# Optimization experiments

Measured on AMD Instinct MI355X. Metric: run time of the kernel, lower is better.

Reference implementation:

```python
import jax, jax.numpy as jnp
import numpy as np

N, K, C, OUT = 2048, 14, 512, 512
SCALE = 4.0
BN_EPS = 1e-5


def _edge_lists(k):
    # pairs i<j with i,j != k-1 and adj[i,j] > 0 (adj is fully connected ones)
    ei, ej = [], []
    for i in range(k - 1):
        for j in range(i + 1, k - 1):
            ei.append(i)
            ej.append(j)
    return np.asarray(ei, np.int32), np.asarray(ej, np.int32)


def setup_inputs() -> dict:
    key = jax.random.key(0)
    k0, k1, k2, k3 = jax.random.split(key, 4)
    ei, ej = _edge_lists(K)
    std = 0.02
    return {
        "inputs": jax.random.normal(k0, (N, K, C), dtype=jnp.float32),
        "adj": jnp.ones((K, K), dtype=jnp.float32),
        "edge_i": jnp.asarray(ei),
        "edge_j": jnp.asarray(ej),
        "gamma": jnp.ones((C,), dtype=jnp.float32),
        "beta": jnp.zeros((C,), dtype=jnp.float32),
        "w_direct": jax.random.normal(k1, (C,), dtype=jnp.float32) * std,
        "W_merged": jax.random.normal(k2, (OUT, C), dtype=jnp.float32) * std,
        "W_orig": jax.random.normal(k3, (OUT, C), dtype=jnp.float32) * std,
    }


def reference(inputs, adj, edge_i, edge_j, gamma, beta, w_direct, W_merged, W_orig):
    n, k, c = inputs.shape
    # --- learn_adj ---
    global_feat = inputs[:, k - 1 : k, :]                      # [N,1,c]
    distances = jnp.abs(inputs - global_feat)                  # [N,k,c]
    # pairwise gaps only on the static edge list (i<j, non-global, adj>0)
    gap = 15.0 * (distances[:, edge_i, :] - distances[:, edge_j, :])  # [N,E,c]
    # BatchNorm1d over channel c, batch stats over (N, E), biased variance
    mean = jnp.mean(gap, axis=(0, 1))
    var = jnp.mean(jnp.square(gap - mean), axis=(0, 1))
    bn = (gap - mean) * (gamma / jnp.sqrt(var + BN_EPS)) + beta        # [N,E,c]
    a = jax.nn.sigmoid(SCALE * jnp.einsum("nec,c->ne", bn, w_direct))  # [N,E]
    adj2 = jnp.ones((n, k, k), dtype=inputs.dtype)
    adj2 = adj2.at[:, edge_i, edge_j].set(2.0 * a)
    adj2 = adj2.at[:, edge_j, edge_i].set(2.0 * (1.0 - a))
    new_adj = adj2 * adj[None, :, :]
    norm = jnp.sum(jnp.abs(new_adj), axis=2, keepdims=True)    # L1 row norm
    new_adj = new_adj / jnp.maximum(norm, 1e-12)
    # --- graph conv ---
    agg = jnp.einsum("nij,njc->nic", new_adj, inputs)          # [N,k,c]
    merged = jax.nn.relu(jnp.einsum("nkc,oc->nko", agg, W_merged))
    original = jnp.einsum("nkc,oc->nko", inputs, W_orig)
    return merged + original
```

## Files before the change

### kernel.cpp

```cpp
#include <hip/hip_runtime.h>
#include <stdint.h>

#define K_NODES 14
#define C_DIM   512
#define OUT_DIM 512
#define N_EDGE  78

typedef float  f32x4  __attribute__((ext_vector_type(4)));
typedef __bf16 bf16x8 __attribute__((ext_vector_type(8)));

__device__ __forceinline__ unsigned short f2bf(float f) {
    unsigned int u = __builtin_bit_cast(unsigned int, f);
    unsigned int r = (u + 0x7fffu + ((u >> 16) & 1u)) >> 16;
    return (unsigned short)r;
}
__device__ __forceinline__ float bf2f(unsigned short s) {
    return __builtin_bit_cast(float, (unsigned int)s << 16);
}

__device__ __forceinline__ void async16(const void* g, void* l) {
    __builtin_amdgcn_global_load_lds(
        (const __attribute__((address_space(1))) unsigned int*)g,
        (__attribute__((address_space(3))) unsigned int*)l, 16, 0, 0);
}

__global__ __launch_bounds__(512) void stats_partial(
    const float* __restrict__ x, float* __restrict__ part,
    unsigned short* __restrict__ xbf,
    const float* __restrict__ Wm, const float* __restrict__ Wo,
    unsigned short* __restrict__ wmbf, unsigned short* __restrict__ wobf)
{
    int t  = threadIdx.x;
    int q  = t & 127;
    int sn = t >> 7;
    f32x4 as = (f32x4){0.f,0.f,0.f,0.f};
    f32x4 aq = (f32x4){0.f,0.f,0.f,0.f};

    #pragma unroll
    for (int half = 0; half < 2; ++half) {
        int n = blockIdx.x * 8 + half * 4 + sn;
        size_t base = (size_t)n * K_NODES * C_DIM + q * 4;

        f32x4 g = *(const f32x4*)(x + base + 13 * C_DIM);
        ushort4 gb; gb.x=f2bf(g.x); gb.y=f2bf(g.y); gb.z=f2bf(g.z); gb.w=f2bf(g.w);
        *(ushort4*)(xbf + base + 13 * C_DIM) = gb;

        float S10=0,S11=0,S12=0,S13=0, S20=0,S21=0,S22=0,S23=0, Sw0=0,Sw1=0,Sw2=0,Sw3=0;
        #pragma unroll
        for (int k = 0; k < 13; ++k) {
            f32x4 v = *(const f32x4*)(x + base + k * C_DIM);
            ushort4 vb; vb.x=f2bf(v.x); vb.y=f2bf(v.y); vb.z=f2bf(v.z); vb.w=f2bf(v.w);
            *(ushort4*)(xbf + base + k * C_DIM) = vb;
            float wk = (float)(12 - 2 * k);
            float d0=fabsf(v.x-g.x), d1=fabsf(v.y-g.y), d2=fabsf(v.z-g.z), d3=fabsf(v.w-g.w);
            S10+=d0; S11+=d1; S12+=d2; S13+=d3;
            S20+=d0*d0; S21+=d1*d1; S22+=d2*d2; S23+=d3*d3;
            Sw0+=wk*d0; Sw1+=wk*d1; Sw2+=wk*d2; Sw3+=wk*d3;
        }
        as += (f32x4){15.f*Sw0, 15.f*Sw1, 15.f*Sw2, 15.f*Sw3};
        aq += (f32x4){225.f*(13.f*S20 - S10*S10), 225.f*(13.f*S21 - S11*S11),
                      225.f*(13.f*S22 - S12*S12), 225.f*(13.f*S23 - S13*S13)};
    }

    __shared__ f32x4 redS[4][128];
    __shared__ f32x4 redQ[4][128];
    redS[sn][q] = as;
    redQ[sn][q] = aq;
    __syncthreads();
    if (sn == 0) {
        f32x4 s = redS[0][q], z = redQ[0][q];
        #pragma unroll
        for (int r = 1; r < 4; ++r) { s += redS[r][q]; z += redQ[r][q]; }
        *(f32x4*)(part + (size_t)blockIdx.x * 1024 + q * 4)       = s;
        *(f32x4*)(part + (size_t)blockIdx.x * 1024 + 512 + q * 4) = z;
    }
    int i0 = blockIdx.x * 1024 + t;
    wmbf[i0] = f2bf(Wm[i0]);
    wobf[i0] = f2bf(Wo[i0]);
    wmbf[i0 + 512] = f2bf(Wm[i0 + 512]);
    wobf[i0 + 512] = f2bf(Wo[i0 + 512]);
}

__global__ __launch_bounds__(256) void finalize_stats(
    const float* __restrict__ part, float inv_ne,
    const float* __restrict__ gamma, const float* __restrict__ beta,
    const float* __restrict__ wdir, float* __restrict__ u, float* __restrict__ bpart)
{
    int lane = threadIdx.x & 63;
    int wv   = threadIdx.x >> 6;
    int c    = blockIdx.x * 64 + lane;
    float s = 0.f, q = 0.f;
    #pragma unroll 8
    for (int r = wv; r < 256; r += 4) {
        s += part[(size_t)r * 1024 + c];
        q += part[(size_t)r * 1024 + 512 + c];
    }
    __shared__ float shs[4][64], shq[4][64];
    shs[wv][lane] = s; shq[wv][lane] = q;
    __syncthreads();
    if (wv == 0) {
        s = shs[0][lane] + shs[1][lane] + shs[2][lane] + shs[3][lane];
        q = shq[0][lane] + shq[1][lane] + shq[2][lane] + shq[3][lane];
        float mean = s * inv_ne;
        float var  = q * inv_ne - mean * mean;
        float sc   = gamma[c] / sqrtf(var + 1e-5f);
        u[c] = sc * wdir[c];
        float b = (beta[c] - mean * sc) * wdir[c];
        #pragma unroll
        for (int off = 1; off < 64; off <<= 1) b += __shfl_xor(b, off, 64);
        if (lane == 0) bpart[blockIdx.x] = b;
    }
}

__global__ __launch_bounds__(256) void fuse_graph(
    const unsigned short* __restrict__ xbf, const float* __restrict__ adj,
    const int* __restrict__ ei, const int* __restrict__ ej,
    const float* __restrict__ u, const float* __restrict__ bpart,
    unsigned short* __restrict__ aggbf)
{
    __shared__ float WL[4][196];
    __shared__ float Dsh[4][13];
    __shared__ float invW[4][14];
    int wv = threadIdx.x >> 6, lane = threadIdx.x & 63;
    int n  = blockIdx.x * 4 + wv;
    size_t base = (size_t)n * K_NODES * C_DIM + lane * 8;

    float xf[K_NODES][8];
    #pragma unroll
    for (int k = 0; k < K_NODES; ++k) {
        uint4 raw = *(const uint4*)(xbf + base + k * C_DIM);
        xf[k][0]=bf2f(raw.x&0xffff); xf[k][1]=bf2f(raw.x>>16);
        xf[k][2]=bf2f(raw.y&0xffff); xf[k][3]=bf2f(raw.y>>16);
        xf[k][4]=bf2f(raw.z&0xffff); xf[k][5]=bf2f(raw.z>>16);
        xf[k][6]=bf2f(raw.w&0xffff); xf[k][7]=bf2f(raw.w>>16);
    }
    float uvv[8];
    {
        f32x4 a = *(const f32x4*)(u + lane * 8);
        f32x4 b = *(const f32x4*)(u + lane * 8 + 4);
        uvv[0]=a.x; uvv[1]=a.y; uvv[2]=a.z; uvv[3]=a.w;
        uvv[4]=b.x; uvv[5]=b.y; uvv[6]=b.z; uvv[7]=b.w;
    }

    #pragma unroll
    for (int k = 0; k < 13; ++k) {
        float p = 0.f;
        #pragma unroll
        for (int c = 0; c < 8; ++c) p += fabsf(xf[k][c]-xf[13][c])*uvv[c];
        #pragma unroll
        for (int off = 1; off < 64; off <<= 1) p += __shfl_xor(p, off, 64);
        if (lane == 0) Dsh[wv][k] = p;
    }

    #pragma unroll
    for (int r = 0; r < 4; ++r) {
        int idx = r * 64 + lane;
        if (idx < K_NODES * K_NODES) {
            int i = idx / K_NODES, j = idx - i * K_NODES;
            if (i == j || i == 13 || j == 13) WL[wv][idx] = adj[idx];
        }
    }
    float bc = 0.f;
    #pragma unroll
    for (int b8 = 0; b8 < 8; ++b8) bc += bpart[b8];
    #pragma unroll
    for (int r = 0; r < 2; ++r) {
        int e = r * 64 + lane;
        if (e < N_EDGE) {
            int ii = ei[e], jj = ej[e];
            float z = 4.0f * (15.f * (Dsh[wv][ii] - Dsh[wv][jj]) + bc);
            float a = 1.f / (1.f + expf(-z));
            WL[wv][ii * K_NODES + jj] = adj[ii * K_NODES + jj] * (2.f * a);
            WL[wv][jj * K_NODES + ii] = adj[jj * K_NODES + ii] * (2.f * (1.f - a));
        }
    }
    if (lane < K_NODES) {
        float s = 0.f;
        #pragma unroll
        for (int j = 0; j < K_NODES; ++j) s += fabsf(WL[wv][lane * K_NODES + j]);
        invW[wv][lane] = 1.f / fmaxf(s, 1e-12f);
    }

    #pragma unroll
    for (int i = 0; i < K_NODES; ++i) {
        float s0=0,s1=0,s2=0,s3=0,s4=0,s5=0,s6=0,s7=0;
        #pragma unroll
        for (int j = 0; j < K_NODES; ++j) {
            float w = WL[wv][i * K_NODES + j];
            s0+=w*xf[j][0]; s1+=w*xf[j][1]; s2+=w*xf[j][2]; s3+=w*xf[j][3];
            s4+=w*xf[j][4]; s5+=w*xf[j][5]; s6+=w*xf[j][6]; s7+=w*xf[j][7];
        }
        float wi = invW[wv][i];
        uint4 r;
        r.x = (unsigned int)f2bf(s0*wi) | ((unsigned int)f2bf(s1*wi) << 16);
        r.y = (unsigned int)f2bf(s2*wi) | ((unsigned int)f2bf(s3*wi) << 16);
        r.z = (unsigned int)f2bf(s4*wi) | ((unsigned int)f2bf(s5*wi) << 16);
        r.w = (unsigned int)f2bf(s6*wi) | ((unsigned int)f2bf(s7*wi) << 16);
        *(uint4*)(aggbf + base + i * C_DIM) = r;
    }
}

#define TM 128
#define TN 128
#define BK 64

__global__ __launch_bounds__(256) void gemm_fused(
    const unsigned short* __restrict__ Aagg, const unsigned short* __restrict__ Axin,
    const unsigned short* __restrict__ Bwm,  const unsigned short* __restrict__ Bwo,
    float* __restrict__ out)
{
    __shared__ unsigned short lA[2][TM * BK];
    __shared__ unsigned short lB[2][TN * BK];
    int tid  = threadIdx.x;
    int lane = tid & 63;
    int wave = tid >> 6;
    int wr = wave >> 1, wc = wave & 1;
    int bm = blockIdx.x * TM;
    int bn = blockIdx.y * TN;

    f32x4 acc[4][4];
    #pragma unroll
    for (int i = 0; i < 4; ++i)
        #pragma unroll
        for (int j = 0; j < 4; ++j) acc[i][j] = (f32x4){0.f, 0.f, 0.f, 0.f};

    int lrow = lane & 15;
    int xorv = lane & 7;
    int srow  = tid >> 3;
    int lcu   = ((tid & 7) ^ (srow & 7)) * 8;

#define STAGE(buf, Ap, Bp, kb)                                              \
    _Pragma("unroll")                                                        \
    for (int it = 0; it < 4; ++it) {                                         \
        int row = it * 32 + srow;                                            \
        async16((Ap) + (size_t)(bm + row) * C_DIM + (kb) + lcu,              \
                &lA[buf][(it * 256 + wave * 64) * 8]);                       \
        async16((Bp) + (size_t)(bn + row) * C_DIM + (kb) + lcu,              \
                &lB[buf][(it * 256 + wave * 64) * 8]);                       \
    }

    STAGE(0, Aagg, Bwm, 0);
    __syncthreads();

    #pragma unroll
    for (int ph = 0; ph < 16; ++ph) {
        const int cur = ph & 1;
        if (ph < 15) {
            const unsigned short* Ap = ((ph + 1) < 8) ? Aagg : Axin;
            const unsigned short* Bp = ((ph + 1) < 8) ? Bwm  : Bwo;
            STAGE(cur ^ 1, Ap, Bp, ((ph + 1) & 7) * BK);
        }
        #pragma unroll
        for (int ks = 0; ks < 2; ++ks) {
            int pchunk = ((ks * 4 + (lane >> 4)) ^ xorv) * 8;
            bf16x8 af[4], bfr[4];
            #pragma unroll
            for (int i = 0; i < 4; ++i)
                af[i] = *(const bf16x8*)&lA[cur][(wr * 64 + i * 16 + lrow) * BK + pchunk];
            #pragma unroll
            for (int j = 0; j < 4; ++j)
                bfr[j] = *(const bf16x8*)&lB[cur][(wc * 64 + j * 16 + lrow) * BK + pchunk];
            #pragma unroll
            for (int i = 0; i < 4; ++i)
                #pragma unroll
                for (int j = 0; j < 4; ++j)
                    acc[i][j] = __builtin_amdgcn_mfma_f32_16x16x32_bf16(
                        af[i], bfr[j], acc[i][j], 0, 0, 0);
        }
        if (ph == 7) {
            #pragma unroll
            for (int i = 0; i < 4; ++i)
                #pragma unroll
                for (int j = 0; j < 4; ++j)
                    #pragma unroll
                    for (int r = 0; r < 4; ++r)
                        acc[i][j][r] = fmaxf(acc[i][j][r], 0.f);
        }
        __syncthreads();
    }
#undef STAGE

    int orow0 = bm + wr * 64 + (lane >> 4) * 4;
    int ocol0 = bn + wc * 64 + (lane & 15);
    #pragma unroll
    for (int i = 0; i < 4; ++i)
        #pragma unroll
        for (int j = 0; j < 4; ++j)
            #pragma unroll
            for (int r = 0; r < 4; ++r)
                out[(size_t)(orow0 + i * 16 + r) * OUT_DIM + (ocol0 + j * 16)] = acc[i][j][r];
}

extern "C" void kernel_launch(void* const* d_in, const int* in_sizes, int n_in,
                              void* d_out, int out_size, void* d_ws, size_t ws_size,
                              hipStream_t stream)
{
    const float* x     = (const float*)d_in[0];
    const float* adj   = (const float*)d_in[1];
    const int*   ei    = (const int*)d_in[2];
    const int*   ej    = (const int*)d_in[3];
    const float* gamma = (const float*)d_in[4];
    const float* beta  = (const float*)d_in[5];
    const float* wdir  = (const float*)d_in[6];
    const float* Wm    = (const float*)d_in[7];
    const float* Wo    = (const float*)d_in[8];
    float* out = (float*)d_out;

    int N = in_sizes[0] / (K_NODES * C_DIM);
    int M = N * K_NODES;

    float* ws_f   = (float*)d_ws;
    float* u      = ws_f + 1024;
    float* bpart  = ws_f + 1536;
    float* part   = ws_f + 2048;
    char*  wsb    = (char*)d_ws;
    size_t off    = (size_t)(2048 + 256 * 1024) * sizeof(float);
    unsigned short* wmbf  = (unsigned short*)(wsb + off);  off += (size_t)OUT_DIM * C_DIM * 2;
    unsigned short* wobf  = (unsigned short*)(wsb + off);  off += (size_t)OUT_DIM * C_DIM * 2;
    unsigned short* xbf   = (unsigned short*)(wsb + off);  off += (size_t)M * C_DIM * 2;
    unsigned short* aggbf = (unsigned short*)(wsb + off);

    float inv_ne = 1.0f / ((float)N * (float)N_EDGE);

    hipLaunchKernelGGL(stats_partial, dim3(N / 8), dim3(512), 0, stream,
                       x, part, xbf, Wm, Wo, wmbf, wobf);
    hipLaunchKernelGGL(finalize_stats, dim3(8), dim3(256), 0, stream,
                       part, inv_ne, gamma, beta, wdir, u, bpart);
    hipLaunchKernelGGL(fuse_graph, dim3(N / 4), dim3(256), 0, stream,
                       xbf, adj, ei, ej, u, bpart, aggbf);
    hipLaunchKernelGGL(gemm_fused, dim3(M / TM, OUT_DIM / TN), dim3(256), 0, stream,
                       aggbf, xbf, wmbf, wobf, out);
}
```

Measured before the change: 183.0 us.

## Apply normalized adjacency after GEMM instead of materializing aggregated features

Reorders the computation so that x·W_merged^T is computed once alongside x·W_orig^T. The per-sample normalized 14x14 adjacency is then applied to the GEMM output in an epilogue before the ReLU. The gate kernel now writes only the normalized adjacency weights instead of a full bf16 aggregated-feature tensor. This removes one full activation write and read and halves the A-operand streaming in the GEMM. In exchange the GEMM uses a 112-row tile with 512 threads and about 120KB of shared memory, and adds an LDS-based epilogue for the small adjacency matmul.

```diff
diff --git a/kernel.cpp b/kernel.cpp
--- a/kernel.cpp
+++ b/kernel.cpp
@@ -112,11 +112,11 @@
     }
 }
 
-__global__ __launch_bounds__(256) void fuse_graph(
+__global__ __launch_bounds__(256) void fuse_gates(
     const unsigned short* __restrict__ xbf, const float* __restrict__ adj,
     const int* __restrict__ ei, const int* __restrict__ ej,
     const float* __restrict__ u, const float* __restrict__ bpart,
-    unsigned short* __restrict__ aggbf)
+    float* __restrict__ wfull)
 {
     __shared__ float WL[4][196];
     __shared__ float Dsh[4][13];
@@ -180,115 +180,132 @@
         for (int j = 0; j < K_NODES; ++j) s += fabsf(WL[wv][lane * K_NODES + j]);
         invW[wv][lane] = 1.f / fmaxf(s, 1e-12f);
     }
-
-    #pragma unroll
-    for (int i = 0; i < K_NODES; ++i) {
-        float s0=0,s1=0,s2=0,s3=0,s4=0,s5=0,s6=0,s7=0;
-        #pragma unroll
-        for (int j = 0; j < K_NODES; ++j) {
-            float w = WL[wv][i * K_NODES + j];
-            s0+=w*xf[j][0]; s1+=w*xf[j][1]; s2+=w*xf[j][2]; s3+=w*xf[j][3];
-            s4+=w*xf[j][4]; s5+=w*xf[j][5]; s6+=w*xf[j][6]; s7+=w*xf[j][7];
-        }
-        float wi = invW[wv][i];
-        uint4 r;
-        r.x = (unsigned int)f2bf(s0*wi) | ((unsigned int)f2bf(s1*wi) << 16);
-        r.y = (unsigned int)f2bf(s2*wi) | ((unsigned int)f2bf(s3*wi) << 16);
-        r.z = (unsigned int)f2bf(s4*wi) | ((unsigned int)f2bf(s5*wi) << 16);
-        r.w = (unsigned int)f2bf(s6*wi) | ((unsigned int)f2bf(s7*wi) << 16);
-        *(uint4*)(aggbf + base + i * C_DIM) = r;
-    }
-}
-
-#define TM 128
+    #pragma unroll
+    for (int r = 0; r < 4; ++r) {
+        int idx = r * 64 + lane;
+        if (idx < 196) {
+            int i = idx / K_NODES;
+            wfull[(size_t)n * 196 + idx] = WL[wv][idx] * invW[wv][i];
+        }
+    }
+}
+
+#define TM 112
 #define TN 128
 #define BK 64
-
-__global__ __launch_bounds__(256) void gemm_fused(
-    const unsigned short* __restrict__ Aagg, const unsigned short* __restrict__ Axin,
+#define NROW 368
+#define NISSUE 46
+
+__global__ __launch_bounds__(512, 2) void gemm_fused(
+    const unsigned short* __restrict__ Axin,
     const unsigned short* __restrict__ Bwm,  const unsigned short* __restrict__ Bwo,
+    const float* __restrict__ wfull,
     float* __restrict__ out)
 {
-    __shared__ unsigned short lA[2][TM * BK];
-    __shared__ unsigned short lB[2][TN * BK];
+    __shared__ __align__(16) char smem[122752];
+    unsigned short (*lS)[NROW * BK] = (unsigned short (*)[NROW * BK])smem;
+
     int tid  = threadIdx.x;
     int lane = tid & 63;
     int wave = tid >> 6;
-    int wr = wave >> 1, wc = wave & 1;
     int bm = blockIdx.x * TM;
     int bn = blockIdx.y * TN;
 
-    f32x4 acc[4][4];
-    #pragma unroll
-    for (int i = 0; i < 4; ++i)
-        #pragma unroll
-        for (int j = 0; j < 4; ++j) acc[i][j] = (f32x4){0.f, 0.f, 0.f, 0.f};
+    const unsigned short* gsrc[6];
+    #pragma unroll
+    for (int k = 0; k < 6; ++k) {
+        int q = wave + k * 8;
+        if (q < NISSUE) {
+            int r   = q * 8 + (lane >> 3);
+            int lch = (lane & 7) ^ (r & 7);
+            const unsigned short* s;
+            if (q < 14)      s = Axin + (size_t)(bm + r) * C_DIM;
+            else if (q < 30) s = Bwm  + (size_t)(bn + r - 112) * C_DIM;
+            else             s = Bwo  + (size_t)(bn + r - 240) * C_DIM;
+            gsrc[k] = s + lch * 8;
+        } else gsrc[k] = Axin;
+    }
+
+#define STAGE(buf, kb)                                                       \
+    _Pragma("unroll")                                                         \
+    for (int k = 0; k < 6; ++k)                                               \
+        if (wave + k * 8 < NISSUE)                                            \
+            async16(gsrc[k] + (kb), &lS[buf][(wave + k * 8) * 512]);
+
+    f32x4 accm[7], acco[7];
+    #pragma unroll
+    for (int i = 0; i < 7; ++i) {
+        accm[i] = (f32x4){0.f,0.f,0.f,0.f};
+        acco[i] = (f32x4){0.f,0.f,0.f,0.f};
+    }
 
     int lrow = lane & 15;
     int xorv = lane & 7;
-    int srow  = tid >> 3;
-    int lcu   = ((tid & 7) ^ (srow & 7)) * 8;
-
-#define STAGE(buf, Ap, Bp, kb)                                              \
-    _Pragma("unroll")                                                        \
-    for (int it = 0; it < 4; ++it) {                                         \
-        int row = it * 32 + srow;                                            \
-        async16((Ap) + (size_t)(bm + row) * C_DIM + (kb) + lcu,              \
-                &lA[buf][(it * 256 + wave * 64) * 8]);                       \
-        async16((Bp) + (size_t)(bn + row) * C_DIM + (kb) + lcu,              \
-                &lB[buf][(it * 256 + wave * 64) * 8]);                       \
-    }
-
-    STAGE(0, Aagg, Bwm, 0);
+
+    STAGE(0, 0)
     __syncthreads();
 
     #pragma unroll
-    for (int ph = 0; ph < 16; ++ph) {
-        const int cur = ph & 1;
-        if (ph < 15) {
-            const unsigned short* Ap = ((ph + 1) < 8) ? Aagg : Axin;
-            const unsigned short* Bp = ((ph + 1) < 8) ? Bwm  : Bwo;
-            STAGE(cur ^ 1, Ap, Bp, ((ph + 1) & 7) * BK);
-        }
+    for (int t = 0; t < 8; ++t) {
+        const int cur = t & 1;
+        if (t < 7) STAGE(cur ^ 1, (t + 1) * BK)
         #pragma unroll
         for (int ks = 0; ks < 2; ++ks) {
-            int pchunk = ((ks * 4 + (lane >> 4)) ^ xorv) * 8;
-            bf16x8 af[4], bfr[4];
+            int pch = ((ks * 4 + (lane >> 4)) ^ xorv) * 8;
+            bf16x8 af[7], bmf, bof;
             #pragma unroll
-            for (int i = 0; i < 4; ++i)
-                af[i] = *(const bf16x8*)&lA[cur][(wr * 64 + i * 16 + lrow) * BK + pchunk];
+            for (int i = 0; i < 7; ++i)
+                af[i] = *(const bf16x8*)&lS[cur][(i * 16 + lrow) * BK + pch];
+            bmf = *(const bf16x8*)&lS[cur][(112 + wave * 16 + lrow) * BK + pch];
+            bof = *(const bf16x8*)&lS[cur][(240 + wave * 16 + lrow) * BK + pch];
             #pragma unroll
-            for (int j = 0; j < 4; ++j)
-                bfr[j] = *(const bf16x8*)&lB[cur][(wc * 64 + j * 16 + lrow) * BK + pchunk];
-            #pragma unroll
-            for (int i = 0; i < 4; ++i)
-                #pragma unroll
-                for (int j = 0; j < 4; ++j)
-                    acc[i][j] = __builtin_amdgcn_mfma_f32_16x16x32_bf16(
-                        af[i], bfr[j], acc[i][j], 0, 0, 0);
-        }
-        if (ph == 7) {
-            #pragma unroll
-            for (int i = 0; i < 4; ++i)
-                #pragma unroll
-                for (int j = 0; j < 4; ++j)
-                    #pragma unroll
-                    for (int r = 0; r < 4; ++r)
-                        acc[i][j][r] = fmaxf(acc[i][j][r], 0.f);
+            for (int i = 0; i < 7; ++i) {
+                accm[i] = __builtin_amdgcn_mfma_f32_16x16x32_bf16(af[i], bmf, accm[i], 0,0,0);
+                acco[i] = __builtin_amdgcn_mfma_f32_16x16x32_bf16(af[i], bof, acco[i], 0,0,0);
+            }
         }
         __syncthreads();
     }
 #undef STAGE
 
-    int orow0 = bm + wr * 64 + (lane >> 4) * 4;
-    int ocol0 = bn + wc * 64 + (lane & 15);
-    #pragma unroll
-    for (int i = 0; i < 4; ++i)
-        #pragma unroll
-        for (int j = 0; j < 4; ++j)
-            #pragma unroll
-            for (int r = 0; r < 4; ++r)
-                out[(size_t)(orow0 + i * 16 + r) * OUT_DIM + (ocol0 + j * 16)] = acc[i][j][r];
+    float (*UmL)[130] = (float (*)[130])smem;
+    float (*UoL)[130] = (float (*)[130])(smem + 58240);
+    float *wsh        = (float*)(smem + 116480);
+
+    int q4 = lane >> 4, c15 = lane & 15;
+    #pragma unroll
+    for (int i = 0; i < 7; ++i)
+        #pragma unroll
+        for (int r = 0; r < 4; ++r) {
+            int row = i * 16 + q4 * 4 + r;
+            UmL[row][wave * 16 + c15] = accm[i][r];
+            UoL[row][wave * 16 + c15] = acco[i][r];
+        }
+    for (int idx = tid; idx < 8 * 196; idx += 512)
+        wsh[idx] = wfull[(size_t)blockIdx.x * 8 * 196 + idx];
+    __syncthreads();
+
+    float a0[14], a1[14];
+    #pragma unroll
+    for (int ii = 0; ii < 14; ++ii) { a0[ii] = 0.f; a1[ii] = 0.f; }
+    #pragma unroll
+    for (int j = 0; j < 14; ++j) {
+        float um0 = UmL[wave * 14 + j][lane];
+        float um1 = UmL[wave * 14 + j][lane + 64];
+        #pragma unroll
+        for (int ii = 0; ii < 14; ++ii) {
+            float wv_ = wsh[wave * 196 + ii * 14 + j];
+            a0[ii] += wv_ * um0;
+            a1[ii] += wv_ * um1;
+        }
+    }
+    #pragma unroll
+    for (int ii = 0; ii < 14; ++ii) {
+        int row = wave * 14 + ii;
+        size_t o = (size_t)(bm + row) * OUT_DIM + bn;
+        out[o + lane]      = fmaxf(a0[ii], 0.f) + UoL[row][lane];
+        out[o + lane + 64] = fmaxf(a1[ii], 0.f) + UoL[row][lane + 64];
+    }
 }
 
 extern "C" void kernel_launch(void* const* d_in, const int* in_sizes, int n_in,
@@ -318,7 +335,7 @@
     unsigned short* wmbf  = (unsigned short*)(wsb + off);  off += (size_t)OUT_DIM * C_DIM * 2;
     unsigned short* wobf  = (unsigned short*)(wsb + off);  off += (size_t)OUT_DIM * C_DIM * 2;
     unsigned short* xbf   = (unsigned short*)(wsb + off);  off += (size_t)M * C_DIM * 2;
-    unsigned short* aggbf = (unsigned short*)(wsb + off);
+    float*          wfull = (float*)(wsb + off);           off += (size_t)N * 196 * 4;
 
     float inv_ne = 1.0f / ((float)N * (float)N_EDGE);
 
@@ -326,8 +343,8 @@
                        x, part, xbf, Wm, Wo, wmbf, wobf);
     hipLaunchKernelGGL(finalize_stats, dim3(8), dim3(256), 0, stream,
                        part, inv_ne, gamma, beta, wdir, u, bpart);
-    hipLaunchKernelGGL(fuse_graph, dim3(N / 4), dim3(256), 0, stream,
-                       xbf, adj, ei, ej, u, bpart, aggbf);
-    hipLaunchKernelGGL(gemm_fused, dim3(M / TM, OUT_DIM / TN), dim3(256), 0, stream,
-                       aggbf, xbf, wmbf, wobf, out);
-}
+    hipLaunchKernelGGL(fuse_gates, dim3(N / 4), dim3(256), 0, stream,
+                       xbf, adj, ei, ej, u, bpart, wfull);
+    hipLaunchKernelGGL(gemm_fused, dim3(M / TM, OUT_DIM / TN), dim3(512), 0, stream,
+                       xbf, wmbf, wobf, wfull, out);
+}
```

After: 185.3 us. About the same (+1.2%).

## Replace stats partials and finalize kernel with atomics and in-kernel finalize

Applied to the files above, without the earlier changes.

The stats kernel now handles 4 samples per block over twice as many blocks and accumulates per-channel sums into a global buffer with float atomics, instead of writing per-block partials. The separate finalize kernel is removed. Every fuse_graph block recomputes the BN scale vector and bias from the accumulated sums into shared memory. This drops one kernel launch and the partial-buffer round trip, but adds a memset, atomic contention on 1024 addresses, redundant per-block finalize work, and order-dependent float accumulation.

```diff
diff --git a/kernel.cpp b/kernel.cpp
--- a/kernel.cpp
+++ b/kernel.cpp
@@ -25,7 +25,7 @@
 }
 
 __global__ __launch_bounds__(512) void stats_partial(
-    const float* __restrict__ x, float* __restrict__ part,
+    const float* __restrict__ x, float* __restrict__ accum,
     unsigned short* __restrict__ xbf,
     const float* __restrict__ Wm, const float* __restrict__ Wo,
     unsigned short* __restrict__ wmbf, unsigned short* __restrict__ wobf)
@@ -33,34 +33,28 @@
     int t  = threadIdx.x;
     int q  = t & 127;
     int sn = t >> 7;
-    f32x4 as = (f32x4){0.f,0.f,0.f,0.f};
-    f32x4 aq = (f32x4){0.f,0.f,0.f,0.f};
-
-    #pragma unroll
-    for (int half = 0; half < 2; ++half) {
-        int n = blockIdx.x * 8 + half * 4 + sn;
-        size_t base = (size_t)n * K_NODES * C_DIM + q * 4;
-
-        f32x4 g = *(const f32x4*)(x + base + 13 * C_DIM);
-        ushort4 gb; gb.x=f2bf(g.x); gb.y=f2bf(g.y); gb.z=f2bf(g.z); gb.w=f2bf(g.w);
-        *(ushort4*)(xbf + base + 13 * C_DIM) = gb;
-
-        float S10=0,S11=0,S12=0,S13=0, S20=0,S21=0,S22=0,S23=0, Sw0=0,Sw1=0,Sw2=0,Sw3=0;
-        #pragma unroll
-        for (int k = 0; k < 13; ++k) {
-            f32x4 v = *(const f32x4*)(x + base + k * C_DIM);
-            ushort4 vb; vb.x=f2bf(v.x); vb.y=f2bf(v.y); vb.z=f2bf(v.z); vb.w=f2bf(v.w);
-            *(ushort4*)(xbf + base + k * C_DIM) = vb;
-            float wk = (float)(12 - 2 * k);
-            float d0=fabsf(v.x-g.x), d1=fabsf(v.y-g.y), d2=fabsf(v.z-g.z), d3=fabsf(v.w-g.w);
-            S10+=d0; S11+=d1; S12+=d2; S13+=d3;
-            S20+=d0*d0; S21+=d1*d1; S22+=d2*d2; S23+=d3*d3;
-            Sw0+=wk*d0; Sw1+=wk*d1; Sw2+=wk*d2; Sw3+=wk*d3;
-        }
-        as += (f32x4){15.f*Sw0, 15.f*Sw1, 15.f*Sw2, 15.f*Sw3};
-        aq += (f32x4){225.f*(13.f*S20 - S10*S10), 225.f*(13.f*S21 - S11*S11),
-                      225.f*(13.f*S22 - S12*S12), 225.f*(13.f*S23 - S13*S13)};
-    }
+    int n  = blockIdx.x * 4 + sn;
+    size_t base = (size_t)n * K_NODES * C_DIM + q * 4;
+
+    f32x4 g = *(const f32x4*)(x + base + 13 * C_DIM);
+    ushort4 gb; gb.x=f2bf(g.x); gb.y=f2bf(g.y); gb.z=f2bf(g.z); gb.w=f2bf(g.w);
+    *(ushort4*)(xbf + base + 13 * C_DIM) = gb;
+
+    float S10=0,S11=0,S12=0,S13=0, S20=0,S21=0,S22=0,S23=0, Sw0=0,Sw1=0,Sw2=0,Sw3=0;
+    #pragma unroll
+    for (int k = 0; k < 13; ++k) {
+        f32x4 v = *(const f32x4*)(x + base + k * C_DIM);
+        ushort4 vb; vb.x=f2bf(v.x); vb.y=f2bf(v.y); vb.z=f2bf(v.z); vb.w=f2bf(v.w);
+        *(ushort4*)(xbf + base + k * C_DIM) = vb;
+        float wk = (float)(12 - 2 * k);
+        float d0=fabsf(v.x-g.x), d1=fabsf(v.y-g.y), d2=fabsf(v.z-g.z), d3=fabsf(v.w-g.w);
+        S10+=d0; S11+=d1; S12+=d2; S13+=d3;
+        S20+=d0*d0; S21+=d1*d1; S22+=d2*d2; S23+=d3*d3;
+        Sw0+=wk*d0; Sw1+=wk*d1; Sw2+=wk*d2; Sw3+=wk*d3;
+    }
+    f32x4 as = (f32x4){15.f*Sw0, 15.f*Sw1, 15.f*Sw2, 15.f*Sw3};
+    f32x4 aq = (f32x4){225.f*(13.f*S20 - S10*S10), 225.f*(13.f*S21 - S11*S11),
+                       225.f*(13.f*S22 - S12*S12), 225.f*(13.f*S23 - S13*S13)};
 
     __shared__ f32x4 redS[4][128];
     __shared__ f32x4 redQ[4][128];
@@ -68,62 +62,55 @@
     redQ[sn][q] = aq;
     __syncthreads();
     if (sn == 0) {
-        f32x4 s = redS[0][q], z = redQ[0][q];
-        #pragma unroll
-        for (int r = 1; r < 4; ++r) { s += redS[r][q]; z += redQ[r][q]; }
-        *(f32x4*)(part + (size_t)blockIdx.x * 1024 + q * 4)       = s;
-        *(f32x4*)(part + (size_t)blockIdx.x * 1024 + 512 + q * 4) = z;
-    }
-    int i0 = blockIdx.x * 1024 + t;
+        f32x4 s = redS[0][q] + redS[1][q] + redS[2][q] + redS[3][q];
+        f32x4 z = redQ[0][q] + redQ[1][q] + redQ[2][q] + redQ[3][q];
+        atomicAdd(&accum[q * 4 + 0], s.x);
+        atomicAdd(&accum[q * 4 + 1], s.y);
+        atomicAdd(&accum[q * 4 + 2], s.z);
+        atomicAdd(&accum[q * 4 + 3], s.w);
+        atomicAdd(&accum[512 + q * 4 + 0], z.x);
+        atomicAdd(&accum[512 + q * 4 + 1], z.y);
+        atomicAdd(&accum[512 + q * 4 + 2], z.z);
+        atomicAdd(&accum[512 + q * 4 + 3], z.w);
+    }
+    int i0 = blockIdx.x * 512 + t;
     wmbf[i0] = f2bf(Wm[i0]);
     wobf[i0] = f2bf(Wo[i0]);
-    wmbf[i0 + 512] = f2bf(Wm[i0 + 512]);
-    wobf[i0 + 512] = f2bf(Wo[i0 + 512]);
-}
-
-__global__ __launch_bounds__(256) void finalize_stats(
-    const float* __restrict__ part, float inv_ne,
-    const float* __restrict__ gamma, const float* __restrict__ beta,
-    const float* __restrict__ wdir, float* __restrict__ u, float* __restrict__ bpart)
-{
-    int lane = threadIdx.x & 63;
-    int wv   = threadIdx.x >> 6;
-    int c    = blockIdx.x * 64 + lane;
-    float s = 0.f, q = 0.f;
-    #pragma unroll 8
-    for (int r = wv; r < 256; r += 4) {
-        s += part[(size_t)r * 1024 + c];
-        q += part[(size_t)r * 1024 + 512 + c];
-    }
-    __shared__ float shs[4][64], shq[4][64];
-    shs[wv][lane] = s; shq[wv][lane] = q;
-    __syncthreads();
-    if (wv == 0) {
-        s = shs[0][lane] + shs[1][lane] + shs[2][lane] + shs[3][lane];
-        q = shq[0][lane] + shq[1][lane] + shq[2][lane] + shq[3][lane];
-        float mean = s * inv_ne;
-        float var  = q * inv_ne - mean * mean;
-        float sc   = gamma[c] / sqrtf(var + 1e-5f);
-        u[c] = sc * wdir[c];
-        float b = (beta[c] - mean * sc) * wdir[c];
-        #pragma unroll
-        for (int off = 1; off < 64; off <<= 1) b += __shfl_xor(b, off, 64);
-        if (lane == 0) bpart[blockIdx.x] = b;
-    }
 }
 
 __global__ __launch_bounds__(256) void fuse_graph(
     const unsigned short* __restrict__ xbf, const float* __restrict__ adj,
     const int* __restrict__ ei, const int* __restrict__ ej,
-    const float* __restrict__ u, const float* __restrict__ bpart,
+    const float* __restrict__ accum,
+    const float* __restrict__ gamma, const float* __restrict__ beta,
+    const float* __restrict__ wdir, float inv_ne,
     unsigned short* __restrict__ aggbf)
 {
+    __shared__ float uS[512];
+    __shared__ float bred[4];
     __shared__ float WL[4][196];
     __shared__ float Dsh[4][13];
     __shared__ float invW[4][14];
-    int wv = threadIdx.x >> 6, lane = threadIdx.x & 63;
+    int tid = threadIdx.x;
+    int wv = tid >> 6, lane = tid & 63;
     int n  = blockIdx.x * 4 + wv;
     size_t base = (size_t)n * K_NODES * C_DIM + lane * 8;
+
+    float bp = 0.f;
+    #pragma unroll
+    for (int c0 = 0; c0 < 512; c0 += 256) {
+        int c = c0 + tid;
+        float s  = accum[c];
+        float qq = accum[512 + c];
+        float mean = s * inv_ne;
+        float var  = qq * inv_ne - mean * mean;
+        float sc   = gamma[c] / sqrtf(var + 1e-5f);
+        uS[c] = sc * wdir[c];
+        bp += (beta[c] - mean * sc) * wdir[c];
+    }
+    #pragma unroll
+    for (int off = 1; off < 64; off <<= 1) bp += __shfl_xor(bp, off, 64);
+    if (lane == 0) bred[wv] = bp;
 
     float xf[K_NODES][8];
     #pragma unroll
@@ -134,13 +121,11 @@
         xf[k][4]=bf2f(raw.z&0xffff); xf[k][5]=bf2f(raw.z>>16);
         xf[k][6]=bf2f(raw.w&0xffff); xf[k][7]=bf2f(raw.w>>16);
     }
+    __syncthreads();
+    float bc = bred[0] + bred[1] + bred[2] + bred[3];
     float uvv[8];
-    {
-        f32x4 a = *(const f32x4*)(u + lane * 8);
-        f32x4 b = *(const f32x4*)(u + lane * 8 + 4);
-        uvv[0]=a.x; uvv[1]=a.y; uvv[2]=a.z; uvv[3]=a.w;
-        uvv[4]=b.x; uvv[5]=b.y; uvv[6]=b.z; uvv[7]=b.w;
-    }
+    #pragma unroll
+    for (int c = 0; c < 8; ++c) uvv[c] = uS[lane * 8 + c];
 
     #pragma unroll
     for (int k = 0; k < 13; ++k) {
@@ -160,9 +145,6 @@
             if (i == j || i == 13 || j == 13) WL[wv][idx] = adj[idx];
         }
     }
-    float bc = 0.f;
-    #pragma unroll
-    for (int b8 = 0; b8 < 8; ++b8) bc += bpart[b8];
     #pragma unroll
     for (int r = 0; r < 2; ++r) {
         int e = r * 64 + lane;
@@ -310,9 +292,7 @@
     int M = N * K_NODES;
 
     float* ws_f   = (float*)d_ws;
-    float* u      = ws_f + 1024;
-    float* bpart  = ws_f + 1536;
-    float* part   = ws_f + 2048;
+    float* accum  = ws_f;
     char*  wsb    = (char*)d_ws;
     size_t off    = (size_t)(2048 + 256 * 1024) * sizeof(float);
     unsigned short* wmbf  = (unsigned short*)(wsb + off);  off += (size_t)OUT_DIM * C_DIM * 2;
@@ -322,12 +302,11 @@
 
     float inv_ne = 1.0f / ((float)N * (float)N_EDGE);
 
-    hipLaunchKernelGGL(stats_partial, dim3(N / 8), dim3(512), 0, stream,
-                       x, part, xbf, Wm, Wo, wmbf, wobf);
-    hipLaunchKernelGGL(finalize_stats, dim3(8), dim3(256), 0, stream,
-                       part, inv_ne, gamma, beta, wdir, u, bpart);
+    hipMemsetAsync(accum, 0, 1024 * sizeof(float), stream);
+    hipLaunchKernelGGL(stats_partial, dim3(N / 4), dim3(512), 0, stream,
+                       x, accum, xbf, Wm, Wo, wmbf, wobf);
     hipLaunchKernelGGL(fuse_graph, dim3(N / 4), dim3(256), 0, stream,
-                       xbf, adj, ei, ej, u, bpart, aggbf);
+                       xbf, adj, ei, ej, accum, gamma, beta, wdir, inv_ne, aggbf);
     hipLaunchKernelGGL(gemm_fused, dim3(M / TM, OUT_DIM / TN), dim3(256), 0, stream,
                        aggbf, xbf, wmbf, wobf, out);
 }
```

Measured after the change: 216.9 us. 18.5% more time.
